# Optimization experiments

Hardware: AMD Instinct MI355X
Metric: run time of the kernel (lower is better)

The kernel has to match this reference:

```python
import jax, jax.numpy as jnp
import numpy as np

N_NODES = 100000
N_EDGES = 1600000
D = 128


def setup_inputs() -> dict:
    key = jax.random.key(0)
    k1, k2, k3 = jax.random.split(key, 3)
    x = jax.random.normal(k1, (N_NODES, D), dtype=jnp.float32)
    edge_index = jax.random.randint(k2, (2, N_EDGES), 0, N_NODES, dtype=jnp.int64)
    weight = jax.random.normal(k3, (D, D), dtype=jnp.float32) * (1.0 / np.sqrt(D))
    bias = jnp.zeros((D,), dtype=jnp.float32)
    return {"x": x, "edge_index": edge_index, "weight": weight, "bias": bias}


def reference(x, edge_index, weight, bias):
    # Eval-mode forward: dropout(p=0.5, training=False) is identity.
    N = x.shape[0]
    row, col = edge_index[0], edge_index[1]  # source -> target

    # gcn_norm: add self loops (weight 1), symmetric normalization
    loop = jnp.arange(N, dtype=edge_index.dtype)
    full_row = jnp.concatenate([row, loop])
    full_col = jnp.concatenate([col, loop])
    ew = jnp.ones(full_row.shape[0], dtype=x.dtype)
    deg = jax.ops.segment_sum(ew, full_col, num_segments=N)
    deg_inv_sqrt = jnp.where(deg > 0, jax.lax.rsqrt(jnp.maximum(deg, 1e-12)), 0.0)
    norm = deg_inv_sqrt[full_row] * ew * deg_inv_sqrt[full_col]  # [E+N]

    # linear transform then gather-scale-scatter aggregation
    h = x @ weight.T  # [N, D]
    msgs = h[full_row] * norm[:, None]  # [E+N, D]
    out = jax.ops.segment_sum(msgs, full_col, num_segments=N)
    out = out + bias
    return jax.nn.relu(out)
```

## Files before the change

### kernel.cpp

```cpp
#include <hip/hip_runtime.h>

#define N_NODES 100000
#define N_EDGES 1600000
#define D 128
#define N_STRIPS (N_NODES / 32)

#define BSH   9
#define NBKT  196
#define P_BLK 160
#define EPB   (N_EDGES / P_BLK)

typedef __bf16 bf16x2 __attribute__((ext_vector_type(2)));
typedef __bf16 bf16x4 __attribute__((ext_vector_type(4)));
typedef __bf16 bf16x8 __attribute__((ext_vector_type(8)));
typedef float  f32x4  __attribute__((ext_vector_type(4)));

__global__ __launch_bounds__(256) void k_cast(const float4* __restrict__ x4,
                                              const float4* __restrict__ w4,
                                              bf16x4* __restrict__ xb4,
                                              bf16x4* __restrict__ wb4) {
    int i = blockIdx.x * 256 + threadIdx.x;
    float4 v = x4[i];
    bf16x4 o;
    o[0] = (__bf16)v.x; o[1] = (__bf16)v.y; o[2] = (__bf16)v.z; o[3] = (__bf16)v.w;
    xb4[i] = o;
    if (i < (D * D) / 4) {
        float4 u = w4[i];
        bf16x4 p;
        p[0] = (__bf16)u.x; p[1] = (__bf16)u.y; p[2] = (__bf16)u.z; p[3] = (__bf16)u.w;
        wb4[i] = p;
    }
}

__global__ __launch_bounds__(1024) void k_bhist(const int* __restrict__ col,
                                                int* __restrict__ bhist) {
    __shared__ int lh[NBKT];
    int tid = threadIdx.x, b = blockIdx.x;
    if (tid < NBKT) lh[tid] = 0;
    __syncthreads();
    int e0 = b * EPB;
    for (int e = e0 + tid; e < e0 + EPB; e += 1024)
        atomicAdd(&lh[col[e] >> BSH], 1);
    __syncthreads();
    if (tid < NBKT) bhist[tid * P_BLK + b] = lh[tid];
}

__global__ __launch_bounds__(256) void k_bscan(int* __restrict__ bhist,
                                               int* __restrict__ gtot) {
    __shared__ int buf[256];
    int k = blockIdx.x, t = threadIdx.x;
    int v = (t < P_BLK) ? bhist[k * P_BLK + t] : 0;
    buf[t] = v;
    __syncthreads();
    for (int off = 1; off < 256; off <<= 1) {
        int u = (t >= off) ? buf[t - off] : 0;
        __syncthreads();
        buf[t] += u;
        __syncthreads();
    }
    if (t < P_BLK) bhist[k * P_BLK + t] = buf[t] - v;
    if (t == 255) gtot[k] = buf[255];
}

__global__ __launch_bounds__(256) void k_gscan(const int* __restrict__ gtot,
                                               int* __restrict__ gstart) {
    __shared__ int buf[256];
    int t = threadIdx.x;
    int v = (t < NBKT) ? gtot[t] : 0;
    buf[t] = v;
    __syncthreads();
    for (int off = 1; off < 256; off <<= 1) {
        int u = (t >= off) ? buf[t - off] : 0;
        __syncthreads();
        buf[t] += u;
        __syncthreads();
    }
    if (t < NBKT) gstart[t] = buf[t] - v;
}

__global__ __launch_bounds__(1024) void k_cscatter(const int* __restrict__ row,
                                                   const int* __restrict__ col,
                                                   const int* __restrict__ bhist,
                                                   const int* __restrict__ gstart,
                                                   unsigned* __restrict__ grec) {
    __shared__ int cur[NBKT];
    int b = blockIdx.x, t = threadIdx.x;
    if (t < NBKT) cur[t] = gstart[t] + bhist[t * P_BLK + b];
    __syncthreads();
    int e0 = b * EPB;
    for (int e = e0 + t; e < e0 + EPB; e += 1024) {
        int c = col[e];
        unsigned rec = ((unsigned)row[e] << BSH) | (unsigned)(c & ((1 << BSH) - 1));
        int pos = atomicAdd(&cur[c >> BSH], 1);
        grec[pos] = rec;
    }
}

__global__ __launch_bounds__(1024) void k_fine(const unsigned* __restrict__ grec,
                                               const int* __restrict__ gtot,
                                               const int* __restrict__ gstart,
                                               int* __restrict__ deg,
                                               float* __restrict__ dis,
                                               int* __restrict__ start,
                                               int* __restrict__ srcs) {
    __shared__ int fh[512];
    __shared__ int fscan[512];
    int b = blockIdx.x;
    int tid = threadIdx.x;
    int cnt = gtot[b];
    int gs = gstart[b];
    if (tid < 512) fh[tid] = 0;
    __syncthreads();
    for (int i = tid; i < cnt; i += 1024)
        atomicAdd(&fh[grec[gs + i] & 511], 1);
    __syncthreads();
    int v = 0;
    if (tid < 512) { v = fh[tid]; fscan[tid] = v; }
    __syncthreads();
    for (int off = 1; off < 512; off <<= 1) {
        int u = 0;
        if (tid < 512 && tid >= off) u = fscan[tid - off];
        __syncthreads();
        if (tid < 512) fscan[tid] += u;
        __syncthreads();
    }
    if (tid < 512) {
        int excl = fscan[tid] - v;
        int node = (b << BSH) + tid;
        if (node < N_NODES) {
            deg[node] = v;
            dis[node] = rsqrtf((float)v + 1.0f);
            start[node] = gs + excl;
        }
        fh[tid] = excl;
    }
    __syncthreads();
    for (int i = tid; i < cnt; i += 1024) {
        unsigned r = grec[gs + i];
        int pos = atomicAdd(&fh[r & 511], 1);
        srcs[gs + pos] = (int)(r >> BSH);
    }
}

__global__ __launch_bounds__(256) void k_aggregate(const int* __restrict__ srcs,
                                                   const int* __restrict__ start,
                                                   const int* __restrict__ deg,
                                                   const __bf16* __restrict__ xb,
                                                   const float* __restrict__ dis,
                                                   float* __restrict__ out) {
    int node = (blockIdx.x * 256 + threadIdx.x) >> 6;
    int lane = threadIdx.x & 63;
    if (node >= N_NODES) return;
    int s = start[node];
    int n = deg[node];
    float dc = dis[node];
    unsigned u0 = ((const unsigned*)(xb + (size_t)node * D))[lane];
    float accx = __uint_as_float(u0 << 16) * dc * dc;
    float accy = __uint_as_float(u0 & 0xFFFF0000u) * dc * dc;

    for (int base = 0; base < n; base += 64) {
        int m = n - base; if (m > 64) m = 64;
        int   src_l = 0;
        float nr_l  = 0.f;
        if (lane < m) {
            src_l = srcs[s + base + lane];
            nr_l  = dis[src_l] * dc;
        }
        int i = 0;
        for (; i + 8 <= m; i += 8) {
            int   sv[8];
            float nv[8];
            unsigned av[8];
            #pragma unroll
            for (int j = 0; j < 8; ++j) {
                sv[j] = __shfl(src_l, i + j);
                nv[j] = __shfl(nr_l, i + j);
            }
            #pragma unroll
            for (int j = 0; j < 8; ++j)
                av[j] = ((const unsigned*)(xb + (size_t)sv[j] * D))[lane];
            #pragma unroll
            for (int j = 0; j < 8; ++j) {
                accx += __uint_as_float(av[j] << 16) * nv[j];
                accy += __uint_as_float(av[j] & 0xFFFF0000u) * nv[j];
            }
        }
        for (; i + 4 <= m; i += 4) {
            int   sv[4];
            float nv[4];
            unsigned av[4];
            #pragma unroll
            for (int j = 0; j < 4; ++j) {
                sv[j] = __shfl(src_l, i + j);
                nv[j] = __shfl(nr_l, i + j);
            }
            #pragma unroll
            for (int j = 0; j < 4; ++j)
                av[j] = ((const unsigned*)(xb + (size_t)sv[j] * D))[lane];
            #pragma unroll
            for (int j = 0; j < 4; ++j) {
                accx += __uint_as_float(av[j] << 16) * nv[j];
                accy += __uint_as_float(av[j] & 0xFFFF0000u) * nv[j];
            }
        }
        for (; i < m; ++i) {
            int   si = __shfl(src_l, i);
            float ni = __shfl(nr_l, i);
            unsigned a = ((const unsigned*)(xb + (size_t)si * D))[lane];
            accx += __uint_as_float(a << 16) * ni;
            accy += __uint_as_float(a & 0xFFFF0000u) * ni;
        }
    }
    float2 r; r.x = accx; r.y = accy;
    ((float2*)(out + (size_t)node * D))[lane] = r;
}

__global__ __launch_bounds__(256) void k_transform(const __bf16* __restrict__ wb,
                                                   const float* __restrict__ bias,
                                                   float* __restrict__ out) {
    int wave = threadIdx.x >> 6;
    int lane = threadIdx.x & 63;
    int strip = blockIdx.x * 4 + wave;
    if (strip >= N_STRIPS) return;
    int m0 = strip * 32;
    int l15 = lane & 15;
    int kq  = lane >> 4;

    bf16x8 a[2][4];
    #pragma unroll
    for (int mt = 0; mt < 2; ++mt) {
        const float* ap = out + (size_t)(m0 + mt * 16 + l15) * D + kq * 8;
        #pragma unroll
        for (int ks = 0; ks < 4; ++ks) {
            float4 lo = *(const float4*)(ap + ks * 32);
            float4 hi = *(const float4*)(ap + ks * 32 + 4);
            bf16x8 t;
            t[0] = (__bf16)lo.x; t[1] = (__bf16)lo.y;
            t[2] = (__bf16)lo.z; t[3] = (__bf16)lo.w;
            t[4] = (__bf16)hi.x; t[5] = (__bf16)hi.y;
            t[6] = (__bf16)hi.z; t[7] = (__bf16)hi.w;
            a[mt][ks] = t;
        }
    }

    f32x4 acc[2][8] = {};
    #pragma unroll
    for (int ks = 0; ks < 4; ++ks) {
        #pragma unroll
        for (int nt = 0; nt < 8; ++nt) {
            bf16x8 b = *(const bf16x8*)(wb + (size_t)(nt * 16 + l15) * D + ks * 32 + kq * 8);
            acc[0][nt] = __builtin_amdgcn_mfma_f32_16x16x32_bf16(a[0][ks], b, acc[0][nt], 0, 0, 0);
            acc[1][nt] = __builtin_amdgcn_mfma_f32_16x16x32_bf16(a[1][ks], b, acc[1][nt], 0, 0, 0);
        }
    }

    #pragma unroll
    for (int nt = 0; nt < 8; ++nt) {
        int colj = nt * 16 + l15;
        float bj = bias[colj];
        #pragma unroll
        for (int mt = 0; mt < 2; ++mt) {
            #pragma unroll
            for (int r = 0; r < 4; ++r) {
                int rowi = m0 + mt * 16 + kq * 4 + r;
                out[(size_t)rowi * D + colj] = fmaxf(acc[mt][nt][r] + bj, 0.f);
            }
        }
    }
}

extern "C" void kernel_launch(void* const* d_in, const int* in_sizes, int n_in,
                              void* d_out, int out_size, void* d_ws, size_t ws_size,
                              hipStream_t stream) {
    const float* x    = (const float*)d_in[0];
    const int*   ei   = (const int*)d_in[1];
    const float* w    = (const float*)d_in[2];
    const float* bias = (const float*)d_in[3];
    float* out = (float*)d_out;

    char* ws = (char*)d_ws;
    int*      deg    = (int*)ws;              ws += N_NODES * 4;
    float*    dis    = (float*)ws;            ws += N_NODES * 4;
    int*      start  = (int*)ws;              ws += N_NODES * 4;
    int*      bhist  = (int*)ws;              ws += NBKT * P_BLK * 4;
    int*      gtot   = (int*)ws;              ws += 256 * 4;
    int*      gstart = (int*)ws;              ws += 256 * 4;
    __bf16*   wb     = (__bf16*)ws;           ws += D * D * 2;
    unsigned* grec   = (unsigned*)ws;         ws += (size_t)N_EDGES * 4;
    int*      srcs   = (int*)ws;              ws += (size_t)N_EDGES * 4;
    __bf16*   xb     = (__bf16*)ws;

    const int* row = ei;
    const int* col = ei + N_EDGES;

    k_cast     <<<(N_NODES * D / 4) / 256, 256, 0, stream>>>(
                   (const float4*)x, (const float4*)w, (bf16x4*)xb, (bf16x4*)wb);
    k_bhist    <<<P_BLK, 1024, 0, stream>>>(col, bhist);
    k_bscan    <<<NBKT, 256, 0, stream>>>(bhist, gtot);
    k_gscan    <<<1, 256, 0, stream>>>(gtot, gstart);
    k_cscatter <<<P_BLK, 1024, 0, stream>>>(row, col, bhist, gstart, grec);
    k_fine     <<<NBKT, 1024, 0, stream>>>(grec, gtot, gstart, deg, dis, start, srcs);
    k_aggregate<<<(N_NODES * 64 + 255) / 256, 256, 0, stream>>>(srcs, start, deg, xb, dis, out);
    k_transform<<<(N_STRIPS + 3) / 4, 256, 0, stream>>>(wb, bias, out);
}
```

Before: 254.1 us.

## Transform before aggregating, pre-scale rows by source norm, drop cast kernel

Reorders the computation to run the dense matmul first. It stores h = x·Wᵀ in bf16, with each row pre-multiplied by its source node's deg^-1/2. The aggregation then just sums gathered bf16 rows and applies the target scale, bias and ReLU in one pass. That removes the separate x-to-bf16 cast kernel, the fp32 intermediate round-trip through the output buffer, and the per-edge dis lookup and multiply. The gather now uses 8-byte loads with two half-waves handling alternating edges, and the weight cast is folded into the histogram kernel as an extra block. The trade-off is that h is rounded to bf16 after the matmul instead of x before it, which changes the numerical error profile.

New measurement: 227.8 us. 10.4% less time.

```diff
diff --git a/kernel.cpp b/kernel.cpp
--- a/kernel.cpp
+++ b/kernel.cpp
@@ -10,32 +10,26 @@
 #define P_BLK 160
 #define EPB   (N_EDGES / P_BLK)
 
-typedef __bf16 bf16x2 __attribute__((ext_vector_type(2)));
 typedef __bf16 bf16x4 __attribute__((ext_vector_type(4)));
 typedef __bf16 bf16x8 __attribute__((ext_vector_type(8)));
 typedef float  f32x4  __attribute__((ext_vector_type(4)));
 
-__global__ __launch_bounds__(256) void k_cast(const float4* __restrict__ x4,
-                                              const float4* __restrict__ w4,
-                                              bf16x4* __restrict__ xb4,
-                                              bf16x4* __restrict__ wb4) {
-    int i = blockIdx.x * 256 + threadIdx.x;
-    float4 v = x4[i];
-    bf16x4 o;
-    o[0] = (__bf16)v.x; o[1] = (__bf16)v.y; o[2] = (__bf16)v.z; o[3] = (__bf16)v.w;
-    xb4[i] = o;
-    if (i < (D * D) / 4) {
-        float4 u = w4[i];
-        bf16x4 p;
-        p[0] = (__bf16)u.x; p[1] = (__bf16)u.y; p[2] = (__bf16)u.z; p[3] = (__bf16)u.w;
-        wb4[i] = p;
-    }
-}
-
-__global__ __launch_bounds__(1024) void k_bhist(const int* __restrict__ col,
-                                                int* __restrict__ bhist) {
+__global__ __launch_bounds__(1024) void k_prep(const int* __restrict__ col,
+                                               const float4* __restrict__ w4,
+                                               int* __restrict__ bhist,
+                                               bf16x4* __restrict__ wb4) {
+    int tid = threadIdx.x, b = blockIdx.x;
+    if (b == P_BLK) {
+        for (int i = tid; i < (D * D) / 4; i += 1024) {
+            float4 u = w4[i];
+            bf16x4 p;
+            p[0] = (__bf16)u.x; p[1] = (__bf16)u.y;
+            p[2] = (__bf16)u.z; p[3] = (__bf16)u.w;
+            wb4[i] = p;
+        }
+        return;
+    }
     __shared__ int lh[NBKT];
-    int tid = threadIdx.x, b = blockIdx.x;
     if (tid < NBKT) lh[tid] = 0;
     __syncthreads();
     int e0 = b * EPB;
@@ -142,82 +136,10 @@
     }
 }
 
-__global__ __launch_bounds__(256) void k_aggregate(const int* __restrict__ srcs,
-                                                   const int* __restrict__ start,
-                                                   const int* __restrict__ deg,
-                                                   const __bf16* __restrict__ xb,
-                                                   const float* __restrict__ dis,
-                                                   float* __restrict__ out) {
-    int node = (blockIdx.x * 256 + threadIdx.x) >> 6;
-    int lane = threadIdx.x & 63;
-    if (node >= N_NODES) return;
-    int s = start[node];
-    int n = deg[node];
-    float dc = dis[node];
-    unsigned u0 = ((const unsigned*)(xb + (size_t)node * D))[lane];
-    float accx = __uint_as_float(u0 << 16) * dc * dc;
-    float accy = __uint_as_float(u0 & 0xFFFF0000u) * dc * dc;
-
-    for (int base = 0; base < n; base += 64) {
-        int m = n - base; if (m > 64) m = 64;
-        int   src_l = 0;
-        float nr_l  = 0.f;
-        if (lane < m) {
-            src_l = srcs[s + base + lane];
-            nr_l  = dis[src_l] * dc;
-        }
-        int i = 0;
-        for (; i + 8 <= m; i += 8) {
-            int   sv[8];
-            float nv[8];
-            unsigned av[8];
-            #pragma unroll
-            for (int j = 0; j < 8; ++j) {
-                sv[j] = __shfl(src_l, i + j);
-                nv[j] = __shfl(nr_l, i + j);
-            }
-            #pragma unroll
-            for (int j = 0; j < 8; ++j)
-                av[j] = ((const unsigned*)(xb + (size_t)sv[j] * D))[lane];
-            #pragma unroll
-            for (int j = 0; j < 8; ++j) {
-                accx += __uint_as_float(av[j] << 16) * nv[j];
-                accy += __uint_as_float(av[j] & 0xFFFF0000u) * nv[j];
-            }
-        }
-        for (; i + 4 <= m; i += 4) {
-            int   sv[4];
-            float nv[4];
-            unsigned av[4];
-            #pragma unroll
-            for (int j = 0; j < 4; ++j) {
-                sv[j] = __shfl(src_l, i + j);
-                nv[j] = __shfl(nr_l, i + j);
-            }
-            #pragma unroll
-            for (int j = 0; j < 4; ++j)
-                av[j] = ((const unsigned*)(xb + (size_t)sv[j] * D))[lane];
-            #pragma unroll
-            for (int j = 0; j < 4; ++j) {
-                accx += __uint_as_float(av[j] << 16) * nv[j];
-                accy += __uint_as_float(av[j] & 0xFFFF0000u) * nv[j];
-            }
-        }
-        for (; i < m; ++i) {
-            int   si = __shfl(src_l, i);
-            float ni = __shfl(nr_l, i);
-            unsigned a = ((const unsigned*)(xb + (size_t)si * D))[lane];
-            accx += __uint_as_float(a << 16) * ni;
-            accy += __uint_as_float(a & 0xFFFF0000u) * ni;
-        }
-    }
-    float2 r; r.x = accx; r.y = accy;
-    ((float2*)(out + (size_t)node * D))[lane] = r;
-}
-
-__global__ __launch_bounds__(256) void k_transform(const __bf16* __restrict__ wb,
-                                                   const float* __restrict__ bias,
-                                                   float* __restrict__ out) {
+__global__ __launch_bounds__(256) void k_hx(const float* __restrict__ x,
+                                            const __bf16* __restrict__ wb,
+                                            const float* __restrict__ dis,
+                                            __bf16* __restrict__ hb) {
     int wave = threadIdx.x >> 6;
     int lane = threadIdx.x & 63;
     int strip = blockIdx.x * 4 + wave;
@@ -229,7 +151,7 @@
     bf16x8 a[2][4];
     #pragma unroll
     for (int mt = 0; mt < 2; ++mt) {
-        const float* ap = out + (size_t)(m0 + mt * 16 + l15) * D + kq * 8;
+        const float* ap = x + (size_t)(m0 + mt * 16 + l15) * D + kq * 8;
         #pragma unroll
         for (int ks = 0; ks < 4; ++ks) {
             float4 lo = *(const float4*)(ap + ks * 32);
@@ -254,18 +176,106 @@
         }
     }
 
+    float dsv[2][4];
+    #pragma unroll
+    for (int mt = 0; mt < 2; ++mt)
+        #pragma unroll
+        for (int r = 0; r < 4; ++r)
+            dsv[mt][r] = dis[m0 + mt * 16 + kq * 4 + r];
+
     #pragma unroll
     for (int nt = 0; nt < 8; ++nt) {
         int colj = nt * 16 + l15;
-        float bj = bias[colj];
         #pragma unroll
         for (int mt = 0; mt < 2; ++mt) {
             #pragma unroll
             for (int r = 0; r < 4; ++r) {
                 int rowi = m0 + mt * 16 + kq * 4 + r;
-                out[(size_t)rowi * D + colj] = fmaxf(acc[mt][nt][r] + bj, 0.f);
+                hb[(size_t)rowi * D + colj] = (__bf16)(acc[mt][nt][r] * dsv[mt][r]);
             }
         }
+    }
+}
+
+__global__ __launch_bounds__(256) void k_aggregate(const int* __restrict__ srcs,
+                                                   const int* __restrict__ start,
+                                                   const int* __restrict__ deg,
+                                                   const __bf16* __restrict__ hb,
+                                                   const float* __restrict__ dis,
+                                                   const float* __restrict__ bias,
+                                                   float* __restrict__ out) {
+    int node = (blockIdx.x * 256 + threadIdx.x) >> 6;
+    int lane = threadIdx.x & 63;
+    if (node >= N_NODES) return;
+    int li   = lane & 31;
+    int half = lane >> 5;
+    int s = start[node];
+    int n = deg[node];
+    float dc = dis[node];
+    const unsigned char* hbase = (const unsigned char*)hb;
+    size_t boff = (size_t)li * 8;
+
+    float acc0 = 0.f, acc1 = 0.f, acc2 = 0.f, acc3 = 0.f;
+
+    for (int base = 0; base < n; base += 64) {
+        int m = n - base; if (m > 64) m = 64;
+        int src_l = (lane < m) ? srcs[s + base + lane] : 0;
+        int i = 0;
+        for (; i + 16 <= m; i += 16) {
+            int sv[8]; uint2 av[8];
+            #pragma unroll
+            for (int j = 0; j < 8; ++j)
+                sv[j] = __shfl(src_l, i + 2 * j + half);
+            #pragma unroll
+            for (int j = 0; j < 8; ++j)
+                av[j] = *(const uint2*)(hbase + ((size_t)sv[j] * 256 + boff));
+            #pragma unroll
+            for (int j = 0; j < 8; ++j) {
+                acc0 += __uint_as_float(av[j].x << 16);
+                acc1 += __uint_as_float(av[j].x & 0xFFFF0000u);
+                acc2 += __uint_as_float(av[j].y << 16);
+                acc3 += __uint_as_float(av[j].y & 0xFFFF0000u);
+            }
+        }
+        for (; i + 2 <= m; i += 2) {
+            int sj = __shfl(src_l, i + half);
+            uint2 a = *(const uint2*)(hbase + ((size_t)sj * 256 + boff));
+            acc0 += __uint_as_float(a.x << 16);
+            acc1 += __uint_as_float(a.x & 0xFFFF0000u);
+            acc2 += __uint_as_float(a.y << 16);
+            acc3 += __uint_as_float(a.y & 0xFFFF0000u);
+        }
+        if (i < m) {
+            int sj = __shfl(src_l, i);
+            if (half == 0) {
+                uint2 a = *(const uint2*)(hbase + ((size_t)sj * 256 + boff));
+                acc0 += __uint_as_float(a.x << 16);
+                acc1 += __uint_as_float(a.x & 0xFFFF0000u);
+                acc2 += __uint_as_float(a.y << 16);
+                acc3 += __uint_as_float(a.y & 0xFFFF0000u);
+            }
+        }
+    }
+
+    acc0 += __shfl_xor(acc0, 32);
+    acc1 += __shfl_xor(acc1, 32);
+    acc2 += __shfl_xor(acc2, 32);
+    acc3 += __shfl_xor(acc3, 32);
+
+    if (half == 0) {
+        uint2 a = *(const uint2*)(hbase + ((size_t)node * 256 + boff));
+        acc0 += __uint_as_float(a.x << 16);
+        acc1 += __uint_as_float(a.x & 0xFFFF0000u);
+        acc2 += __uint_as_float(a.y << 16);
+        acc3 += __uint_as_float(a.y & 0xFFFF0000u);
+
+        float4 b4 = *(const float4*)(bias + li * 4);
+        float4 r;
+        r.x = fmaxf(acc0 * dc + b4.x, 0.f);
+        r.y = fmaxf(acc1 * dc + b4.y, 0.f);
+        r.z = fmaxf(acc2 * dc + b4.z, 0.f);
+        r.w = fmaxf(acc3 * dc + b4.w, 0.f);
+        *(float4*)(out + (size_t)node * D + li * 4) = r;
     }
 }
 
@@ -288,18 +298,16 @@
     __bf16*   wb     = (__bf16*)ws;           ws += D * D * 2;
     unsigned* grec   = (unsigned*)ws;         ws += (size_t)N_EDGES * 4;
     int*      srcs   = (int*)ws;              ws += (size_t)N_EDGES * 4;
-    __bf16*   xb     = (__bf16*)ws;
+    __bf16*   hb     = (__bf16*)ws;
 
     const int* row = ei;
     const int* col = ei + N_EDGES;
 
-    k_cast     <<<(N_NODES * D / 4) / 256, 256, 0, stream>>>(
-                   (const float4*)x, (const float4*)w, (bf16x4*)xb, (bf16x4*)wb);
-    k_bhist    <<<P_BLK, 1024, 0, stream>>>(col, bhist);
+    k_prep     <<<P_BLK + 1, 1024, 0, stream>>>(col, (const float4*)w, bhist, (bf16x4*)wb);
     k_bscan    <<<NBKT, 256, 0, stream>>>(bhist, gtot);
     k_gscan    <<<1, 256, 0, stream>>>(gtot, gstart);
     k_cscatter <<<P_BLK, 1024, 0, stream>>>(row, col, bhist, gstart, grec);
     k_fine     <<<NBKT, 1024, 0, stream>>>(grec, gtot, gstart, deg, dis, start, srcs);
-    k_aggregate<<<(N_NODES * 64 + 255) / 256, 256, 0, stream>>>(srcs, start, deg, xb, dis, out);
-    k_transform<<<(N_STRIPS + 3) / 4, 256, 0, stream>>>(wb, bias, out);
-}
+    k_hx       <<<(N_STRIPS + 3) / 4, 256, 0, stream>>>(x, wb, dis, hb);
+    k_aggregate<<<(N_NODES * 64 + 255) / 256, 256, 0, stream>>>(srcs, start, deg, hb, dis, bias, out);
+}
```
